# Kernel optimization log

Hardware: AMD Instinct MI355X
Metric: run time of the kernel (lower is better)

The kernel has to match this reference:

```python
import jax, jax.numpy as jnp
import numpy as np

L, B, T, I, H, P, O = 2, 64, 512, 512, 512, 256, 512


def setup_inputs() -> dict:
    key = jax.random.key(0)
    ks = iter(jax.random.split(key, 40))
    SCALE = 0.03  # keep gate pre-activations in a sane range

    def w(shape):
        return jax.random.normal(next(ks), shape, jnp.float32) * SCALE

    return {
        "x": jax.random.normal(next(ks), (B, T, I), jnp.float32),
        "Wr": w((L, H, I + H)), "br": jnp.zeros((L, H), jnp.float32),
        "Wu": w((L, H, I + H)), "bu": jnp.ones((L, H), jnp.float32),  # update_gate bias init to 1.0
        "Wn": w((L, H, I + H)), "bn": jnp.zeros((L, H), jnp.float32),
        "Wmr": w((L, P, H)), "bmr": jnp.zeros((L, P), jnp.float32),
        "Wmw": w((L, P, H)), "bmw": jnp.zeros((L, P), jnp.float32),
        "Wmu": w((L, P, H)), "bmu": jnp.zeros((L, P), jnp.float32),
        "Wmh": w((L, H, P)), "bmh": jnp.zeros((L, H), jnp.float32),
        "Wd": w((L, P, H)), "bd": jnp.zeros((L, P), jnp.float32),
        "Ws": w((L, P, H)), "bs": jnp.zeros((L, P), jnp.float32),
        "Wout": w((O, H)), "bout": jnp.zeros((O,), jnp.float32),
        "dopamine": jnp.full((1,), 0.5, jnp.float32),
        "serotonin": jnp.full((1,), 0.5, jnp.float32),
    }


def _lin(x, W, b):
    # x: [B, in], W: [out, in] (torch Linear layout), b: [out]
    return jnp.einsum("bi,oi->bo", x, W) + b


def reference(x, Wr, br, Wu, bu, Wn, bn, Wmr, bmr, Wmw, bmw, Wmu, bmu,
              Wmh, bmh, Wd, bd, Ws, bs, Wout, bout, dopamine, serotonin):
    num_layers = Wr.shape[0]
    bsz = x.shape[0]
    hdim = Wr.shape[1]
    pdim = Wmr.shape[1]
    h0 = jnp.zeros((num_layers, bsz, hdim), x.dtype)
    m0 = jnp.zeros((num_layers, bsz, pdim), x.dtype)

    def step(carry, x_t):
        hidden, memory = carry  # [L,B,H], [L,B,P]
        inp = x_t
        new_h, new_m = [], []
        for l in range(num_layers):
            h, m = hidden[l], memory[l]
            comb = jnp.concatenate([inp, h], axis=-1)
            reset = jax.nn.sigmoid(_lin(comb, Wr[l], br[l]))
            update = jax.nn.sigmoid(_lin(comb, Wu[l], bu[l]))
            comb_r = jnp.concatenate([inp, reset * h], axis=-1)
            new_hid = jnp.tanh(_lin(comb_r, Wn[l], bn[l]))
            h_cand = (1.0 - update) * h + update * new_hid
            read_gate = jax.nn.sigmoid(_lin(h_cand, Wmr[l], bmr[l]))
            mem_out = read_gate * m
            h_mem = h_cand + _lin(mem_out, Wmh[l], bmh[l])
            write_gate = jax.nn.sigmoid(_lin(h_mem, Wmw[l], bmw[l]))
            new_mem_content = jnp.tanh(_lin(h_mem, Wmu[l], bmu[l]))
            dopa = jax.nn.sigmoid(_lin(h_mem, Wd[l], bd[l]) * dopamine)
            write_gate = write_gate * dopa
            sero = jax.nn.sigmoid(_lin(h_mem, Ws[l], bs[l]) * serotonin)
            write_gate = write_gate * (1.0 - sero)
            m_new = (1.0 - write_gate) * m + write_gate * new_mem_content
            inp = h_mem
            new_h.append(h_mem)
            new_m.append(m_new)
        out_t = _lin(inp, Wout, bout)  # [B, O]
        return (jnp.stack(new_h), jnp.stack(new_m)), out_t

    (h_final, m_final), outs = jax.lax.scan(step, (h0, m0), jnp.swapaxes(x, 0, 1))
    outputs = jnp.swapaxes(outs, 0, 1)  # [B, T, O]
    return outputs, h_final, m_final
```

## Files before the change

### kernel.cpp

```cpp
#include <hip/hip_runtime.h>
#include <math.h>

#define BB 64
#define TT 512
#define II 512
#define HH 512
#define PP 256
#define OO 512

#define NBLK 256
#define NTHR 1024
#define RPB 8
#define AGT __HIP_MEMORY_SCOPE_AGENT

__device__ __align__(256) double g_h0d[2*BB*HH];
__device__ __align__(256) double g_h1 [BB*HH];
__device__ __align__(256) double g_rh [2*BB*HH];
__device__ __align__(256) double g_hc [2*BB*HH];
__device__ __align__(256) double g_mo [2*BB*PP];
__device__ __align__(256) double g_hist[(long)BB*TT*HH];
__device__ unsigned g_sync[4096];

__device__ __align__(256) float g_WRU [2*1024*1024];
__device__ __align__(256) float g_WnT2[2*512*1024];
__device__ __align__(256) float g_WMG [2*512*1024];
__device__ __align__(256) float g_WmrT[2*512*256];
__device__ __align__(256) float g_WmhT[2*256*512];
__device__ __align__(256) float g_WoutT[512*512];

struct KP {
  const float *x,*Wr,*br,*Wu,*bu,*Wn,*bn,*Wmr,*bmr,*Wmw,*bmw,*Wmu,*bmu,
              *Wmh,*bmh,*Wd,*bd,*Ws,*bs,*Wout,*bout,*dop,*ser;
  float* out;
};

__device__ inline double sigd(double x){ return 1.0/(1.0+exp(-x)); }

__global__ void __launch_bounds__(256) prep(KP p)
{
  __shared__ float tile[32][33];
  const int b = blockIdx.x;
  const int T_RUN = 3072;
  const int T_MG  = T_RUN + 1024;
  const int T_MR  = T_MG  + 256;
  const int T_MH  = T_MR  + 256;
  const int T_OUT = T_MH  + 256;
  const int tid = threadIdx.x;

  const float* src=nullptr; float* dst=nullptr;
  int K=0,C=0,st=1,off=0,k0=0,c0=0,mode=0;
  bool xpose=true;

  if (b < T_RUN){
    int m=b>>10, r=b&1023, l=r>>9, t=r&511;
    K=1024; C=512; int ct=t&15, kt=t>>4; k0=kt*32; c0=ct*32;
    src = (m==0? p.Wr : m==1? p.Wu : p.Wn) + (long)l*C*K;
    if (m<2){ dst = g_WRU + (long)l*1024*1024; st=2; off=m; }
    else    { dst = g_WnT2 + (long)l*512*1024; mode=1; }
  } else if (b < T_MG){
    int q=b-T_RUN, m=q>>8, r=q&255, l=r>>7, t=r&127;
    K=512; C=256; int ct=t&7, kt=t>>3; k0=kt*32; c0=ct*32;
    const float* s4[4]={p.Wmw,p.Wmu,p.Wd,p.Ws};
    src = s4[m] + (long)l*C*K;
    dst = g_WMG + (long)l*512*1024; st=4; off=m;
  } else if (b < T_MR){
    int r=b-T_MG, l=r>>7, t=r&127;
    K=512; C=256; int ct=t&7, kt=t>>3; k0=kt*32; c0=ct*32;
    src = p.Wmr + (long)l*C*K;
    dst = g_WmrT + (long)l*512*256; st=1; off=0;
  } else if (b < T_MH){
    int r=b-T_MR, l=r>>7, t=r&127;
    K=256; C=512; int ct=t&15, kt=t>>4; k0=kt*32; c0=ct*32;
    src = p.Wmh + (long)l*C*K;
    dst = g_WmhT + (long)l*256*512; st=1; off=0;
  } else if (b < T_OUT){
    int t=b-T_MH;
    K=512; C=512; int ct=t&15, kt=t>>4; k0=kt*32; c0=ct*32;
    src = p.Wout; dst = g_WoutT; st=1; off=0;
  } else {
    xpose=false;
    long i = (long)(b-T_OUT)*256 + tid;
    if (i < 2L*BB*HH) g_h0d[i]=0.0;
    if (i < (long)BB*HH) g_h1[i]=0.0;
    if (i < 4096) g_sync[(int)i]=0u;
  }

  if (xpose){
    for (int i=tid;i<1024;i+=256){
      int ty=i>>5, tx=i&31;
      tile[ty][tx] = src[(long)(c0+ty)*K + k0+tx];
    }
    __syncthreads();
    for (int i=tid;i<1024;i+=256){
      int ky=i>>5, cx=i&31;
      int k=k0+ky, c=c0+cx;
      long o = mode ? ((long)(k>>1)*1024 + (long)c*2 + (k&1))
                    : ((long)k*C*st + (long)c*st + off);
      dst[o] = tile[cx][ky];
    }
  }
}

__global__ void __launch_bounds__(NTHR,4) rnn_kernel(KP p)
{
  const int tid=threadIdx.x;
  const int xcd=blockIdx.x&7, lay=xcd>>2, xl=xcd&3;
  const int cs=(blockIdx.x>>3)&3, rb=blockIdx.x>>5;
  const int iw=tid>>6, lane=tid&63;
  const int r0g=rb*RPB;
  const int colH0=xl*128+cs*32, colP0=xl*64+cs*16;
  const int cW  = colH0 + (iw>>1)*4;
  const int rset= (iw&1)*4;
  const int cW2 = colH0 + iw*2;
  const int pW  = colP0 + iw;

  __shared__ double sP[RPB][528];
  __shared__ double sH[RPB][528];
  __shared__ double sB[RPB][528];
  __shared__ double sM[RPB][265];
  __shared__ double su[RPB][32];
  __shared__ double sm[RPB][16];

  if (tid<128) sm[tid>>4][tid&15]=0.0;

  auto fs=[](int k){ return k + ((k>>6)<<1); };

  const float* WRU = g_WRU  + (long)lay*1024*1024;
  const float* WN2 = g_WnT2 + (long)lay*512*1024;
  const float* WMGp= g_WMG  + (long)lay*512*1024;
  const float* WMR = g_WmrT + (long)lay*512*256;
  const float* WMH = g_WmhT + (long)lay*256*512;
  const float* br_ = p.br + lay*HH; const float* bu_ = p.bu + lay*HH;
  const float* bn_ = p.bn + lay*HH; const float* bmh_= p.bmh+ lay*HH;
  const float* bmr_= p.bmr+ lay*PP; const float* bmw_= p.bmw+ lay*PP;
  const float* bmu_= p.bmu+ lay*PP; const float* bd_ = p.bd + lay*PP;
  const float* bs_ = p.bs + lay*PP;
  const double dopa = (double)p.dop[0];
  const double sero = (double)p.ser[0];

  double* rhG = g_rh + (long)lay*BB*HH + (long)r0g*HH;
  double* hcG = g_hc + (long)lay*BB*HH + (long)r0g*HH;
  double* moG = g_mo + (long)lay*BB*PP + (long)r0g*PP;

  const int gidx = rb*2 + lay;
  auto bar=[&](int s){
    __syncthreads();
    if (tid==0){
      unsigned* cnt=&g_sync[(gidx*4+s)*32];
      unsigned* gen=cnt+16;
      unsigned ge=__hip_atomic_load(gen,__ATOMIC_RELAXED,AGT);
      unsigned old=__hip_atomic_fetch_add(cnt,1u,__ATOMIC_RELEASE,AGT);
      if (old==15u){
        __hip_atomic_store(cnt,0u,__ATOMIC_RELAXED,AGT);
        __hip_atomic_fetch_add(gen,1u,__ATOMIC_RELEASE,AGT);
      } else {
        while(__hip_atomic_load(gen,__ATOMIC_RELAXED,AGT)==ge) __builtin_amdgcn_s_sleep(1);
      }
      asm volatile("" ::: "memory");
    }
    __syncthreads();
  };
  auto wait_ge=[&](int l,int s,unsigned v){
    if (tid==0){
      unsigned* gen=&g_sync[((rb*2+l)*4+s)*32+16];
      while(__hip_atomic_load(gen,__ATOMIC_RELAXED,AGT)<v) __builtin_amdgcn_s_sleep(1);
      asm volatile("" ::: "memory");
    }
    __syncthreads();
  };

  auto ld512=[&](double dst[RPB][528], const double* src){
    double v[4];
    #pragma unroll
    for (int j=0;j<4;++j){
      int idx=j*1024+tid;
      v[j]=__hip_atomic_load(src + (long)(idx>>9)*HH + (idx&511), __ATOMIC_RELAXED, AGT);
    }
    #pragma unroll
    for (int j=0;j<4;++j){
      int idx=j*1024+tid; int c=idx&511;
      dst[idx>>9][c + ((c>>6)<<1)] = v[j];
    }
  };
  auto ld256=[&](const double* src){
    double v[2];
    #pragma unroll
    for (int j=0;j<2;++j){
      int idx=j*1024+tid;
      v[j]=__hip_atomic_load(src + (long)(idx>>8)*PP + (idx&255), __ATOMIC_RELAXED, AGT);
    }
    #pragma unroll
    for (int j=0;j<2;++j){
      int idx=j*1024+tid; int c=idx&255;
      sM[idx>>8][c + ((c>>6)<<1)] = v[j];
    }
  };
  auto ldX=[&](int t){
    float v[4];
    #pragma unroll
    for (int j=0;j<4;++j){
      int idx=j*1024+tid;
      v[j]=p.x[((long)(r0g+(idx>>9))*TT + t)*II + (idx&511)];
    }
    #pragma unroll
    for (int j=0;j<4;++j){
      int idx=j*1024+tid; int c=idx&511;
      sP[idx>>9][c + ((c>>6)<<1)] = (double)v[j];
    }
  };

  auto ruS=[&](){
    const int c=lane&3, ks=lane>>2;
    const int col=cW+c;
    const float* w = WRU + (long)(ks*64)*1024 + col*2;
    const double* a = (ks<8)? &sP[rset][66*ks] : &sH[rset][66*(ks-8)];
    double ar[4]={0,0,0,0}, au[4]={0,0,0,0};
    #pragma unroll 4
    for (int k=0;k<64;k+=2){
      float2 w0=*(const float2*)(w + (long)k*1024);
      float2 w1=*(const float2*)(w + (long)(k+1)*1024);
      double wr0=(double)w0.x, wu0=(double)w0.y;
      double wr1=(double)w1.x, wu1=(double)w1.y;
      #pragma unroll
      for (int j=0;j<4;++j){
        double2 av=*(const double2*)(a + j*528 + k);
        ar[j]=fma(av.x,wr0,ar[j]); au[j]=fma(av.x,wu0,au[j]);
        ar[j]=fma(av.y,wr1,ar[j]); au[j]=fma(av.y,wu1,au[j]);
      }
    }
    #pragma unroll
    for (int j=0;j<4;++j){
      ar[j]+=__shfl_xor(ar[j],4);  au[j]+=__shfl_xor(au[j],4);
      ar[j]+=__shfl_xor(ar[j],8);  au[j]+=__shfl_xor(au[j],8);
      ar[j]+=__shfl_xor(ar[j],16); au[j]+=__shfl_xor(au[j],16);
      ar[j]+=__shfl_xor(ar[j],32); au[j]+=__shfl_xor(au[j],32);
    }
    if (lane<4){
      const int colw=cW+lane;
      #pragma unroll
      for (int j=0;j<4;++j){
        double r=sigd(ar[j]+(double)br_[colw]);
        double u=sigd(au[j]+(double)bu_[colw]);
        su[rset+j][(iw>>1)*4+lane]=u;
        __hip_atomic_store(&rhG[(long)(rset+j)*HH+colw], r*sH[rset+j][fs(colw)], __ATOMIC_RELAXED, AGT);
      }
    }
  };
  auto nS=[&](){
    const int c=lane&3, ks=lane>>2;
    const int col=cW+c;
    const float* w = WN2 + (long)(ks*32)*1024 + col*2;
    const double* a = (ks<8)? &sP[rset][66*ks] : &sB[rset][66*(ks-8)];
    double ac[4]={0,0,0,0};
    #pragma unroll 4
    for (int kp=0;kp<32;++kp){
      float2 wv=*(const float2*)(w + (long)kp*1024);
      double w0=(double)wv.x, w1=(double)wv.y;
      #pragma unroll
      for (int j=0;j<4;++j){
        double2 av=*(const double2*)(a + j*528 + kp*2);
        ac[j]=fma(av.x,w0,ac[j]); ac[j]=fma(av.y,w1,ac[j]);
      }
    }
    #pragma unroll
    for (int j=0;j<4;++j){
      ac[j]+=__shfl_xor(ac[j],4);  ac[j]+=__shfl_xor(ac[j],8);
      ac[j]+=__shfl_xor(ac[j],16); ac[j]+=__shfl_xor(ac[j],32);
    }
    if (lane<4){
      const int colw=cW+lane;
      #pragma unroll
      for (int j=0;j<4;++j){
        double nh=tanh(ac[j]+(double)bn_[colw]);
        double u=su[rset+j][(iw>>1)*4+lane];
        __hip_atomic_store(&hcG[(long)(rset+j)*HH+colw],
          (1.0-u)*sH[rset+j][fs(colw)]+u*nh, __ATOMIC_RELAXED, AGT);
      }
    }
  };
  auto mgS=[&](){
    const int j=lane&7, ks=lane>>3;
    const float* w4 = WMGp + (long)(ks*64)*1024 + pW*4;
    const double* a = &sH[j][66*ks];
    double q0=0,q1=0,q2=0,q3=0;
    #pragma unroll 4
    for (int k=0;k<64;++k){
      double av=a[k];
      float4 v=*(const float4*)(w4 + (long)k*1024);
      q0=fma(av,(double)v.x,q0); q1=fma(av,(double)v.y,q1);
      q2=fma(av,(double)v.z,q2); q3=fma(av,(double)v.w,q3);
    }
    q0+=__shfl_xor(q0,8); q0+=__shfl_xor(q0,16); q0+=__shfl_xor(q0,32);
    q1+=__shfl_xor(q1,8); q1+=__shfl_xor(q1,16); q1+=__shfl_xor(q1,32);
    q2+=__shfl_xor(q2,8); q2+=__shfl_xor(q2,16); q2+=__shfl_xor(q2,32);
    q3+=__shfl_xor(q3,8); q3+=__shfl_xor(q3,16); q3+=__shfl_xor(q3,32);
    if (lane<8){
      double wg=sigd(q0+(double)bmw_[pW]);
      double nm=tanh(q1+(double)bmu_[pW]);
      double dp=sigd((q2+(double)bd_[pW])*dopa);
      double sr=sigd((q3+(double)bs_[pW])*sero);
      double ww=wg*dp*(1.0-sr);
      sm[lane][iw]=(1.0-ww)*sm[lane][iw]+ww*nm;
    }
  };
  auto rgS=[&](){
    const int j=lane&7, ks=lane>>3;
    const float* w = WMR + (long)(ks*64)*256 + pW;
    const double* a = &sB[j][66*ks];
    double o=0,o2=0;
    #pragma unroll 8
    for (int k=0;k<64;k+=2){
      o =fma(a[k],  (double)w[(long)k*256],    o);
      o2=fma(a[k+1],(double)w[(long)(k+1)*256],o2);
    }
    o+=o2; o+=__shfl_xor(o,8); o+=__shfl_xor(o,16); o+=__shfl_xor(o,32);
    if (lane<8){
      __hip_atomic_store(&moG[(long)lane*PP+pW],
        sigd(o+(double)bmr_[pW])*sm[lane][iw], __ATOMIC_RELAXED, AGT);
    }
  };
  auto hmS=[&](int t){
    const int c=lane&1, j=(lane>>1)&7, ks=lane>>4;
    const int col=cW2+c;
    const float* w = WMH + (long)(ks*64)*512 + col;
    const double* a = &sM[j][66*ks];
    double o=0,o2=0;
    #pragma unroll 8
    for (int k=0;k<64;k+=2){
      o =fma(a[k],  (double)w[(long)k*512],    o);
      o2=fma(a[k+1],(double)w[(long)(k+1)*512],o2);
    }
    o+=o2; o+=__shfl_xor(o,16); o+=__shfl_xor(o,32);
    if (lane<16){
      double hv = o + (double)bmh_[col] + sB[j][fs(col)];
      long gi=(long)(r0g+j)*HH+col;
      if (lay==0){
        __hip_atomic_store(&g_h0d[(long)(t&1)*BB*HH+gi],hv,__ATOMIC_RELAXED,AGT);
      } else {
        __hip_atomic_store(&g_h1[gi],hv,__ATOMIC_RELAXED,AGT);
        __builtin_nontemporal_store(hv,&g_hist[((long)(r0g+j)*TT+t)*HH+col]);
      }
    }
  };

  for (int t=0; t<TT; ++t){
    if (lay==0){
      ldX(t);
      ld512(sH, &g_h0d[(long)((t+1)&1)*BB*HH + (long)r0g*HH]);
    } else {
      wait_ge(0,3,(unsigned)(t+1));
      ld512(sP, &g_h0d[(long)(t&1)*BB*HH + (long)r0g*HH]);
      ld512(sH, g_h1 + (long)r0g*HH);
    }
    __syncthreads();
    ruS();
    if (t>0) mgS();
    bar(0);
    ld512(sB, rhG);
    __syncthreads();
    nS();
    bar(1);
    ld512(sB, hcG);
    __syncthreads();
    rgS();
    bar(2);
    ld256(moG);
    __syncthreads();
    if (lay==0 && t>=2) wait_ge(1,0,(unsigned)(t-1));
    hmS(t);
    bar(3);
  }

  if (lay==0) ld512(sH, &g_h0d[(long)((TT-1)&1)*BB*HH + (long)r0g*HH]);
  else        ld512(sH, g_h1 + (long)r0g*HH);
  __syncthreads();
  mgS();
  __syncthreads();

  const long ob=(long)BB*TT*OO;
  if (tid<256){
    int r=tid>>5, c=tid&31; int col=colH0+c; long bq=r0g+r;
    p.out[ob + (long)lay*BB*HH + bq*HH + col] = (float)sH[r][fs(col)];
  }
  if (tid<128){
    int r=tid>>4, pc=tid&15; int pcol=colP0+pc; long bq=r0g+r;
    p.out[ob + 2L*BB*HH + (long)lay*BB*PP + bq*PP + pcol] = (float)sm[r][pc];
  }
}

__global__ void __launch_bounds__(512) out_gemm(const float* bout, float* out)
{
  __shared__ double sH[8][512];
  const int tid = threadIdx.x;
  const int iw = tid >> 6, lane = tid & 63;
  const int kq = lane >> 5, c32 = lane & 31;
  const int col = iw*64 + c32*2;
  const float* w = g_WoutT + kq*(256*512) + col;
  for (int rbx = blockIdx.x; rbx < BB*TT/8; rbx += gridDim.x){
    __syncthreads();
    for (int i = tid; i < 8*256; i += 512){
      int rr = i >> 8, c2 = (i & 255) << 1;
      *(double2*)&sH[rr][c2] = *(const double2*)(g_hist + (long)(rbx*8+rr)*HH + c2);
    }
    __syncthreads();
    double s[8][2];
    #pragma unroll
    for (int r=0;r<8;++r){ s[r][0]=0.0; s[r][1]=0.0; }
    #pragma unroll 2
    for (int k=0;k<256;++k){
      float2 wv = *(const float2*)(w + (long)k*512);
      double wx = (double)wv.x, wy = (double)wv.y;
      #pragma unroll
      for (int r=0;r<8;++r){
        double av = sH[r][kq*256 + k];
        s[r][0] = fma(av, wx, s[r][0]);
        s[r][1] = fma(av, wy, s[r][1]);
      }
    }
    #pragma unroll
    for (int r=0;r<8;++r){
      double t0 = s[r][0] + __shfl_xor(s[r][0],32);
      double t1 = s[r][1] + __shfl_xor(s[r][1],32);
      if (lane < 32){
        float2 fv;
        fv.x = (float)(t0 + (double)bout[col]);
        fv.y = (float)(t1 + (double)bout[col+1]);
        *(float2*)&out[(long)(rbx*8+r)*OO + col] = fv;
      }
    }
  }
}

extern "C" void kernel_launch(void* const* d_in, const int* in_sizes, int n_in,
                              void* d_out, int out_size, void* d_ws, size_t ws_size,
                              hipStream_t stream)
{
  KP p;
  p.x   = (const float*)d_in[0];
  p.Wr  = (const float*)d_in[1];  p.br  = (const float*)d_in[2];
  p.Wu  = (const float*)d_in[3];  p.bu  = (const float*)d_in[4];
  p.Wn  = (const float*)d_in[5];  p.bn  = (const float*)d_in[6];
  p.Wmr = (const float*)d_in[7];  p.bmr = (const float*)d_in[8];
  p.Wmw = (const float*)d_in[9];  p.bmw = (const float*)d_in[10];
  p.Wmu = (const float*)d_in[11]; p.bmu = (const float*)d_in[12];
  p.Wmh = (const float*)d_in[13]; p.bmh = (const float*)d_in[14];
  p.Wd  = (const float*)d_in[15]; p.bd  = (const float*)d_in[16];
  p.Ws  = (const float*)d_in[17]; p.bs  = (const float*)d_in[18];
  p.Wout= (const float*)d_in[19]; p.bout= (const float*)d_in[20];
  p.dop = (const float*)d_in[21]; p.ser = (const float*)d_in[22];
  p.out = (float*)d_out;

  prep<<<dim3(5120), dim3(256), 0, stream>>>(p);
  rnn_kernel<<<dim3(NBLK), dim3(NTHR), 0, stream>>>(p);
  out_gemm<<<dim3(2048), dim3(512), 0, stream>>>(p.bout, p.out);
}
```

Baseline: 67.16 ms.

## Pad transposed weight row strides and remap RU/N work to 8 columns x 2 rows

Transposed weight buffers get padded row strides (1040, 272, 528 instead of powers of two), meant to cut cache and channel conflicts when many lanes read strided weight rows. The reset/update and candidate matvecs are remapped so each wave handles 8 columns by 2 rows with a 128-long K split, instead of 4 columns by 4 rows. This lowers the per-wave accumulator count and shuffle-reduction steps. Shared-memory activation padding changes from every 64 to every 128 elements, which may bring back some LDS bank conflicts in exchange for fewer wasted slots.

Result: slower. 74.03 ms (+10.2%).

```diff
diff --git a/kernel.cpp b/kernel.cpp
--- a/kernel.cpp
+++ b/kernel.cpp
@@ -12,6 +12,12 @@
 #define NTHR 1024
 #define RPB 8
 #define AGT __HIP_MEMORY_SCOPE_AGENT
+
+#define RS_RU 1040
+#define RS_N  1040
+#define RS_MG 1040
+#define RS_MR 272
+#define RS_MH 528
 
 __device__ __align__(256) double g_h0d[2*BB*HH];
 __device__ __align__(256) double g_h1 [BB*HH];
@@ -21,11 +27,11 @@
 __device__ __align__(256) double g_hist[(long)BB*TT*HH];
 __device__ unsigned g_sync[4096];
 
-__device__ __align__(256) float g_WRU [2*1024*1024];
-__device__ __align__(256) float g_WnT2[2*512*1024];
-__device__ __align__(256) float g_WMG [2*512*1024];
-__device__ __align__(256) float g_WmrT[2*512*256];
-__device__ __align__(256) float g_WmhT[2*256*512];
+__device__ __align__(256) float g_WRU [2*1024*RS_RU];
+__device__ __align__(256) float g_WnT2[2*512*RS_N];
+__device__ __align__(256) float g_WMG [2*512*RS_MG];
+__device__ __align__(256) float g_WmrT[2*512*RS_MR];
+__device__ __align__(256) float g_WmhT[2*256*RS_MH];
 __device__ __align__(256) float g_WoutT[512*512];
 
 struct KP {
@@ -48,35 +54,35 @@
   const int tid = threadIdx.x;
 
   const float* src=nullptr; float* dst=nullptr;
-  int K=0,C=0,st=1,off=0,k0=0,c0=0,mode=0;
+  int K=0,rs=512,st=1,off=0,k0=0,c0=0,mode=0;
   bool xpose=true;
 
   if (b < T_RUN){
     int m=b>>10, r=b&1023, l=r>>9, t=r&511;
-    K=1024; C=512; int ct=t&15, kt=t>>4; k0=kt*32; c0=ct*32;
-    src = (m==0? p.Wr : m==1? p.Wu : p.Wn) + (long)l*C*K;
-    if (m<2){ dst = g_WRU + (long)l*1024*1024; st=2; off=m; }
-    else    { dst = g_WnT2 + (long)l*512*1024; mode=1; }
+    K=1024; int ct=t&15, kt=t>>4; k0=kt*32; c0=ct*32;
+    src = (m==0? p.Wr : m==1? p.Wu : p.Wn) + (long)l*512*1024;
+    if (m<2){ dst = g_WRU + (long)l*1024*RS_RU; rs=RS_RU; st=2; off=m; }
+    else    { dst = g_WnT2 + (long)l*512*RS_N; mode=1; }
   } else if (b < T_MG){
     int q=b-T_RUN, m=q>>8, r=q&255, l=r>>7, t=r&127;
-    K=512; C=256; int ct=t&7, kt=t>>3; k0=kt*32; c0=ct*32;
+    K=512; int ct=t&7, kt=t>>3; k0=kt*32; c0=ct*32;
     const float* s4[4]={p.Wmw,p.Wmu,p.Wd,p.Ws};
-    src = s4[m] + (long)l*C*K;
-    dst = g_WMG + (long)l*512*1024; st=4; off=m;
+    src = s4[m] + (long)l*256*512;
+    dst = g_WMG + (long)l*512*RS_MG; rs=RS_MG; st=4; off=m;
   } else if (b < T_MR){
     int r=b-T_MG, l=r>>7, t=r&127;
-    K=512; C=256; int ct=t&7, kt=t>>3; k0=kt*32; c0=ct*32;
-    src = p.Wmr + (long)l*C*K;
-    dst = g_WmrT + (long)l*512*256; st=1; off=0;
+    K=512; int ct=t&7, kt=t>>3; k0=kt*32; c0=ct*32;
+    src = p.Wmr + (long)l*256*512;
+    dst = g_WmrT + (long)l*512*RS_MR; rs=RS_MR; st=1; off=0;
   } else if (b < T_MH){
     int r=b-T_MR, l=r>>7, t=r&127;
-    K=256; C=512; int ct=t&15, kt=t>>4; k0=kt*32; c0=ct*32;
-    src = p.Wmh + (long)l*C*K;
-    dst = g_WmhT + (long)l*256*512; st=1; off=0;
+    K=256; int ct=t&15, kt=t>>4; k0=kt*32; c0=ct*32;
+    src = p.Wmh + (long)l*512*256;
+    dst = g_WmhT + (long)l*256*RS_MH; rs=RS_MH; st=1; off=0;
   } else if (b < T_OUT){
     int t=b-T_MH;
-    K=512; C=512; int ct=t&15, kt=t>>4; k0=kt*32; c0=ct*32;
-    src = p.Wout; dst = g_WoutT; st=1; off=0;
+    K=512; int ct=t&15, kt=t>>4; k0=kt*32; c0=ct*32;
+    src = p.Wout; dst = g_WoutT; rs=512; st=1; off=0;
   } else {
     xpose=false;
     long i = (long)(b-T_OUT)*256 + tid;
@@ -94,8 +100,8 @@
     for (int i=tid;i<1024;i+=256){
       int ky=i>>5, cx=i&31;
       int k=k0+ky, c=c0+cx;
-      long o = mode ? ((long)(k>>1)*1024 + (long)c*2 + (k&1))
-                    : ((long)k*C*st + (long)c*st + off);
+      long o = mode ? ((long)(k>>1)*RS_N + (long)c*2 + (k&1))
+                    : ((long)k*rs + (long)c*st + off);
       dst[o] = tile[cx][ky];
     }
   }
@@ -109,27 +115,26 @@
   const int iw=tid>>6, lane=tid&63;
   const int r0g=rb*RPB;
   const int colH0=xl*128+cs*32, colP0=xl*64+cs*16;
-  const int cW  = colH0 + (iw>>1)*4;
-  const int rset= (iw&1)*4;
+  const int cg=iw&3, rp=iw>>2;
   const int cW2 = colH0 + iw*2;
   const int pW  = colP0 + iw;
 
-  __shared__ double sP[RPB][528];
-  __shared__ double sH[RPB][528];
-  __shared__ double sB[RPB][528];
+  __shared__ double sP[RPB][520];
+  __shared__ double sH[RPB][520];
+  __shared__ double sB[RPB][520];
   __shared__ double sM[RPB][265];
   __shared__ double su[RPB][32];
   __shared__ double sm[RPB][16];
 
   if (tid<128) sm[tid>>4][tid&15]=0.0;
 
-  auto fs=[](int k){ return k + ((k>>6)<<1); };
-
-  const float* WRU = g_WRU  + (long)lay*1024*1024;
-  const float* WN2 = g_WnT2 + (long)lay*512*1024;
-  const float* WMGp= g_WMG  + (long)lay*512*1024;
-  const float* WMR = g_WmrT + (long)lay*512*256;
-  const float* WMH = g_WmhT + (long)lay*256*512;
+  auto fs=[](int k){ return k + ((k>>7)<<1); };
+
+  const float* WRU = g_WRU  + (long)lay*1024*RS_RU;
+  const float* WN2 = g_WnT2 + (long)lay*512*RS_N;
+  const float* WMGp= g_WMG  + (long)lay*512*RS_MG;
+  const float* WMR = g_WmrT + (long)lay*512*RS_MR;
+  const float* WMH = g_WmhT + (long)lay*256*RS_MH;
   const float* br_ = p.br + lay*HH; const float* bu_ = p.bu + lay*HH;
   const float* bn_ = p.bn + lay*HH; const float* bmh_= p.bmh+ lay*HH;
   const float* bmr_= p.bmr+ lay*PP; const float* bmw_= p.bmw+ lay*PP;
@@ -169,7 +174,7 @@
     __syncthreads();
   };
 
-  auto ld512=[&](double dst[RPB][528], const double* src){
+  auto ld512=[&](double dst[RPB][520], const double* src){
     double v[4];
     #pragma unroll
     for (int j=0;j<4;++j){
@@ -179,7 +184,7 @@
     #pragma unroll
     for (int j=0;j<4;++j){
       int idx=j*1024+tid; int c=idx&511;
-      dst[idx>>9][c + ((c>>6)<<1)] = v[j];
+      dst[idx>>9][c + ((c>>7)<<1)] = v[j];
     }
   };
   auto ld256=[&](const double* src){
@@ -205,88 +210,88 @@
     #pragma unroll
     for (int j=0;j<4;++j){
       int idx=j*1024+tid; int c=idx&511;
-      sP[idx>>9][c + ((c>>6)<<1)] = (double)v[j];
+      sP[idx>>9][c + ((c>>7)<<1)] = (double)v[j];
     }
   };
 
   auto ruS=[&](){
-    const int c=lane&3, ks=lane>>2;
-    const int col=cW+c;
-    const float* w = WRU + (long)(ks*64)*1024 + col*2;
-    const double* a = (ks<8)? &sP[rset][66*ks] : &sH[rset][66*(ks-8)];
-    double ar[4]={0,0,0,0}, au[4]={0,0,0,0};
-    #pragma unroll 4
-    for (int k=0;k<64;k+=2){
-      float2 w0=*(const float2*)(w + (long)k*1024);
-      float2 w1=*(const float2*)(w + (long)(k+1)*1024);
+    const int c=lane&7, ks=lane>>3;
+    const int col=colH0+cg*8+c;
+    const float* w = WRU + (long)(ks*128)*RS_RU + col*2;
+    const double* a = ((ks<4)? &sP[0][130*ks] : &sH[0][130*(ks-4)]) + (rp*2)*520;
+    double ar[2]={0,0}, au[2]={0,0};
+    #pragma unroll 8
+    for (int k=0;k<128;k+=2){
+      float2 w0=*(const float2*)(w + (long)k*RS_RU);
+      float2 w1=*(const float2*)(w + (long)(k+1)*RS_RU);
       double wr0=(double)w0.x, wu0=(double)w0.y;
       double wr1=(double)w1.x, wu1=(double)w1.y;
       #pragma unroll
-      for (int j=0;j<4;++j){
-        double2 av=*(const double2*)(a + j*528 + k);
+      for (int j=0;j<2;++j){
+        double2 av=*(const double2*)(a + j*520 + k);
         ar[j]=fma(av.x,wr0,ar[j]); au[j]=fma(av.x,wu0,au[j]);
         ar[j]=fma(av.y,wr1,ar[j]); au[j]=fma(av.y,wu1,au[j]);
       }
     }
     #pragma unroll
-    for (int j=0;j<4;++j){
-      ar[j]+=__shfl_xor(ar[j],4);  au[j]+=__shfl_xor(au[j],4);
+    for (int j=0;j<2;++j){
       ar[j]+=__shfl_xor(ar[j],8);  au[j]+=__shfl_xor(au[j],8);
       ar[j]+=__shfl_xor(ar[j],16); au[j]+=__shfl_xor(au[j],16);
       ar[j]+=__shfl_xor(ar[j],32); au[j]+=__shfl_xor(au[j],32);
     }
-    if (lane<4){
-      const int colw=cW+lane;
+    if (lane<8){
+      const int colw=colH0+cg*8+lane;
       #pragma unroll
-      for (int j=0;j<4;++j){
+      for (int j=0;j<2;++j){
+        int row=rp*2+j;
         double r=sigd(ar[j]+(double)br_[colw]);
         double u=sigd(au[j]+(double)bu_[colw]);
-        su[rset+j][(iw>>1)*4+lane]=u;
-        __hip_atomic_store(&rhG[(long)(rset+j)*HH+colw], r*sH[rset+j][fs(colw)], __ATOMIC_RELAXED, AGT);
+        su[row][cg*8+lane]=u;
+        __hip_atomic_store(&rhG[(long)row*HH+colw], r*sH[row][fs(colw)], __ATOMIC_RELAXED, AGT);
       }
     }
   };
   auto nS=[&](){
-    const int c=lane&3, ks=lane>>2;
-    const int col=cW+c;
-    const float* w = WN2 + (long)(ks*32)*1024 + col*2;
-    const double* a = (ks<8)? &sP[rset][66*ks] : &sB[rset][66*(ks-8)];
-    double ac[4]={0,0,0,0};
-    #pragma unroll 4
-    for (int kp=0;kp<32;++kp){
-      float2 wv=*(const float2*)(w + (long)kp*1024);
+    const int c=lane&7, ks=lane>>3;
+    const int col=colH0+cg*8+c;
+    const float* w = WN2 + (long)(ks*64)*RS_N + col*2;
+    const double* a = ((ks<4)? &sP[0][130*ks] : &sB[0][130*(ks-4)]) + (rp*2)*520;
+    double ac[2]={0,0};
+    #pragma unroll 8
+    for (int kp=0;kp<64;++kp){
+      float2 wv=*(const float2*)(w + (long)kp*RS_N);
       double w0=(double)wv.x, w1=(double)wv.y;
       #pragma unroll
-      for (int j=0;j<4;++j){
-        double2 av=*(const double2*)(a + j*528 + kp*2);
+      for (int j=0;j<2;++j){
+        double2 av=*(const double2*)(a + j*520 + kp*2);
         ac[j]=fma(av.x,w0,ac[j]); ac[j]=fma(av.y,w1,ac[j]);
       }
     }
     #pragma unroll
-    for (int j=0;j<4;++j){
-      ac[j]+=__shfl_xor(ac[j],4);  ac[j]+=__shfl_xor(ac[j],8);
-      ac[j]+=__shfl_xor(ac[j],16); ac[j]+=__shfl_xor(ac[j],32);
-    }
-    if (lane<4){
-      const int colw=cW+lane;
+    for (int j=0;j<2;++j){
+      ac[j]+=__shfl_xor(ac[j],8); ac[j]+=__shfl_xor(ac[j],16); ac[j]+=__shfl_xor(ac[j],32);
+    }
+    if (lane<8){
+      const int colw=colH0+cg*8+lane;
       #pragma unroll
-      for (int j=0;j<4;++j){
+      for (int j=0;j<2;++j){
+        int row=rp*2+j;
         double nh=tanh(ac[j]+(double)bn_[colw]);
-        double u=su[rset+j][(iw>>1)*4+lane];
-        __hip_atomic_store(&hcG[(long)(rset+j)*HH+colw],
-          (1.0-u)*sH[rset+j][fs(colw)]+u*nh, __ATOMIC_RELAXED, AGT);
+        double u=su[row][cg*8+lane];
+        __hip_atomic_store(&hcG[(long)row*HH+colw],
+          (1.0-u)*sH[row][fs(colw)]+u*nh, __ATOMIC_RELAXED, AGT);
       }
     }
   };
   auto mgS=[&](){
     const int j=lane&7, ks=lane>>3;
-    const float* w4 = WMGp + (long)(ks*64)*1024 + pW*4;
-    const double* a = &sH[j][66*ks];
+    const float* w4 = WMGp + (long)(ks*64)*RS_MG + pW*4;
+    const double* a = &sH[j][64*ks + ((ks>>1)<<1)];
     double q0=0,q1=0,q2=0,q3=0;
     #pragma unroll 4
     for (int k=0;k<64;++k){
       double av=a[k];
-      float4 v=*(const float4*)(w4 + (long)k*1024);
+      float4 v=*(const float4*)(w4 + (long)k*RS_MG);
       q0=fma(av,(double)v.x,q0); q1=fma(av,(double)v.y,q1);
       q2=fma(av,(double)v.z,q2); q3=fma(av,(double)v.w,q3);
     }
@@ -305,13 +310,13 @@
   };
   auto rgS=[&](){
     const int j=lane&7, ks=lane>>3;
-    const float* w = WMR + (long)(ks*64)*256 + pW;
-    const double* a = &sB[j][66*ks];
+    const float* w = WMR + (long)(ks*64)*RS_MR + pW;
+    const double* a = &sB[j][64*ks + ((ks>>1)<<1)];
     double o=0,o2=0;
     #pragma unroll 8
     for (int k=0;k<64;k+=2){
-      o =fma(a[k],  (double)w[(long)k*256],    o);
-      o2=fma(a[k+1],(double)w[(long)(k+1)*256],o2);
+      o =fma(a[k],  (double)w[(long)k*RS_MR],    o);
+      o2=fma(a[k+1],(double)w[(long)(k+1)*RS_MR],o2);
     }
     o+=o2; o+=__shfl_xor(o,8); o+=__shfl_xor(o,16); o+=__shfl_xor(o,32);
     if (lane<8){
@@ -322,13 +327,13 @@
   auto hmS=[&](int t){
     const int c=lane&1, j=(lane>>1)&7, ks=lane>>4;
     const int col=cW2+c;
-    const float* w = WMH + (long)(ks*64)*512 + col;
+    const float* w = WMH + (long)(ks*64)*RS_MH + col;
     const double* a = &sM[j][66*ks];
     double o=0,o2=0;
     #pragma unroll 8
     for (int k=0;k<64;k+=2){
-      o =fma(a[k],  (double)w[(long)k*512],    o);
-      o2=fma(a[k+1],(double)w[(long)(k+1)*512],o2);
+      o =fma(a[k],  (double)w[(long)k*RS_MH],    o);
+      o2=fma(a[k+1],(double)w[(long)(k+1)*RS_MH],o2);
     }
     o+=o2; o+=__shfl_xor(o,16); o+=__shfl_xor(o,32);
     if (lane<16){
```
